# Performance work log

Measured on AMD Instinct MI355X. Metric: run time of the kernel, lower is better.

Reference implementation:

```python
import jax, jax.numpy as jnp
import numpy as np

# ---- st-moe constants (training-mode routing) ----
EPS = 1e-9
TOP_N = 2
CAP_FACTOR = 1.25      # capacity_factor_train
THRESHOLD = 0.2        # threshold_train (2nd expert)
BAL_COEF = 0.01
Z_COEF = 0.001
MIN_CAP = 4
LN_EPS = 1e-5

B, N, D, E = 4, 2048, 512, 8
H = int(D * 4 * 2 / 3)  # 1365, st-moe default Expert hidden


def _rms_norm(x, gamma):
    # F.normalize(x, dim=-1) * sqrt(d) * gamma
    nrm = jnp.maximum(jnp.linalg.norm(x, axis=-1, keepdims=True), 1e-12)
    return x / nrm * (x.shape[-1] ** 0.5) * gamma


def setup_inputs() -> dict:
    key = jax.random.key(0)
    ks = jax.random.split(key, 6)
    s = 0.02
    return {
        "x": jax.random.normal(ks[0], (B, N, D), jnp.float32),
        "gate_w": jax.random.normal(ks[1], (D, E), jnp.float32) * s,
        "prenorm_g": jnp.ones((D,), jnp.float32),
        "w1": jax.random.normal(ks[2], (E, D, 2 * H), jnp.float32) * s,
        "b1": jnp.zeros((E, 2 * H), jnp.float32),
        "mult_bias": jnp.ones((E, H), jnp.float32),
        "w2": jax.random.normal(ks[3], (E, H, D), jnp.float32) * s,
        "b2": jnp.zeros((E, D), jnp.float32),
        "ln_g": jnp.ones((D,), jnp.float32),
        "ln_b": jnp.zeros((D,), jnp.float32),
    }


def _stmoe_fnn(x, gate_w, prenorm_g, w1, b1, mult_bias, w2, b2, ln_g, ln_b):
    b, n, d = x.shape
    e = gate_w.shape[1]
    cap = max(MIN_CAP, min(n, int(n * CAP_FACTOR / e)))  # static python int

    # SparseMoEBlock: moe(RMSNorm(x)) + x
    xg = _rms_norm(x, prenorm_g)

    # ---- TopNGating ----
    gate_logits = jnp.einsum('bnd,de->bne', xg, gate_w)
    raw_gates = jax.nn.softmax(gate_logits, axis=-1)
    gates, idx = jax.lax.top_k(raw_gates, TOP_N)          # (b,n,k)
    gates = jnp.moveaxis(gates, -1, 0)                    # (k,b,n)
    idx = jnp.moveaxis(idx, -1, 0)                        # (k,b,n)
    one_hot = jax.nn.one_hot(idx, e, dtype=x.dtype)       # (k,b,n,e)

    denom = jnp.maximum(gates.sum(axis=0), EPS)
    gates = gates / denom                                 # normalized top-n scores

    # stochastic routing to non-first experts: prob = min(1, gate/threshold)
    thresh = jnp.array([EPS, THRESHOLD], x.dtype)[:, None, None]
    probs = jax.random.uniform(jax.random.key(42), gates.shape, x.dtype)
    should_route = probs < (gates / jnp.maximum(thresh, EPS))
    should_route = should_route.at[0].set(True)
    mask = one_hot * should_route[..., None].astype(x.dtype)  # (k,b,n,e)

    # exclusive cumsum over sequence -> position within each expert
    mask_cumsum = jnp.cumsum(mask, axis=-2) - mask

    positions, kept_masks = [], []
    prev_count = jnp.zeros((b, 1, e), x.dtype)
    for k in range(TOP_N):  # top_n=2, tiny static loop
        pos_in_expert = (mask_cumsum[k] + prev_count) * mask[k]      # (b,n,e)
        kept = mask[k] * (pos_in_expert < float(cap)).astype(x.dtype)
        prev_count = prev_count + kept.sum(axis=-2, keepdims=True)
        positions.append(pos_in_expert.sum(axis=-1))                 # (b,n)
        kept_masks.append(kept)
    mask = jnp.stack(kept_masks)       # (k,b,n,e) post-capacity
    positions = jnp.stack(positions)   # (k,b,n)

    mask_flat = mask.sum(axis=-1)      # (k,b,n)
    gates = gates * mask_flat

    # safe one-hot: out-of-range (overflow) positions map to all-zeros
    pos_one_hot = jax.nn.one_hot(positions.astype(jnp.int32), cap, dtype=x.dtype)  # (k,b,n,c)
    combine = jnp.einsum('kbn,kbne,kbnc->bnec', gates, one_hot, pos_one_hot)       # (b,n,e,c)

    # straight-through dispatch tensor
    dispatch = (combine > 0).astype(x.dtype) + combine - jax.lax.stop_gradient(combine)

    # ---- dispatch, expert GEGLU FFN, combine ----
    expert_in = jnp.einsum('bnd,bnec->becd', xg, dispatch)                 # (b,e,c,d)
    h = jnp.einsum('becd,edf->becf', expert_in, w1) + b1[None, :, None, :]
    u, g = jnp.split(h, 2, axis=-1)
    act = u * jax.nn.gelu(g, approximate=False) * mult_bias[None, :, None, :]
    expert_out = jnp.einsum('bech,ehd->becd', act, w2) + b2[None, :, None, :]
    moe_out = jnp.einsum('becd,bnec->bnd', expert_out, combine)

    # ---- aux losses (training mode) ----
    density_1 = mask[0].mean(axis=-2)          # (b,e), post-capacity mask (torch in-place view)
    density_proxy = raw_gates.mean(axis=-2)    # (b,e)
    balance_loss = (density_proxy * density_1).mean() * float(e ** 2)
    z = jax.nn.logsumexp(gate_logits, axis=-1)
    router_z_loss = jnp.mean(z * z)
    total_aux = BAL_COEF * balance_loss + Z_COEF * router_z_loss

    # residual, (dropout -> identity for determinism), LayerNorm
    y = moe_out + x
    mu = y.mean(axis=-1, keepdims=True)
    var = jnp.mean((y - mu) ** 2, axis=-1, keepdims=True)
    out = (y - mu) * jax.lax.rsqrt(var + LN_EPS) * ln_g + ln_b
    return out, total_aux


def reference(x, gate_w, prenorm_g, w1, b1, mult_bias, w2, b2, ln_g, ln_b):
    return _stmoe_fnn(x, gate_w, prenorm_g, w1, b1, mult_bias, w2, b2, ln_g, ln_b)
```

## Files before the change

kernel.cpp:

```cpp
#include <hip/hip_runtime.h>
#include <hip/hip_bf16.h>
#include <math.h>

#define BB 4
#define NN 2048
#define DD 512
#define EE 8
#define HH 1365
#define H2 2730
#define CAP 320
#define NT (BB*NN)
#define KP2 1408
#define NW1 2816
#define ME 1280
#define KS1 16
#define KS2 44

typedef __bf16 bf16_t;
typedef __bf16 bf16x4 __attribute__((ext_vector_type(4)));
typedef __bf16 bf16x8 __attribute__((ext_vector_type(8)));
typedef float f32x4 __attribute__((ext_vector_type(4)));

__device__ __forceinline__ float gelu_exact(float x){
    return 0.5f * x * (1.0f + erff(x * 0.70710678118654752f));
}
__device__ __forceinline__ void gl2lds16(const void* g, void* s){
    __builtin_amdgcn_global_load_lds((const __attribute__((address_space(1))) unsigned int*)g,
                                     (__attribute__((address_space(3))) unsigned int*)s,
                                     16, 0, 0);
}
__device__ __forceinline__ unsigned rotl32(unsigned x, int d){ return (x<<d)|(x>>(32-d)); }
__device__ __forceinline__ void tf_round(unsigned &x0, unsigned &x1, int r){
    x0 += x1; x1 = rotl32(x1, r); x1 ^= x0;
}
__device__ float threefry_u01_second(unsigned t){
    const unsigned ks0 = 0u, ks1 = 42u, ks2 = 0x1BD11BDAu ^ 42u;
    unsigned x0 = t, x1 = t + 8192u;
    x0 += ks0; x1 += ks1;
    tf_round(x0,x1,13); tf_round(x0,x1,15); tf_round(x0,x1,26); tf_round(x0,x1,6);
    x0 += ks1; x1 += ks2 + 1u;
    tf_round(x0,x1,17); tf_round(x0,x1,29); tf_round(x0,x1,16); tf_round(x0,x1,24);
    x0 += ks2; x1 += ks0 + 2u;
    tf_round(x0,x1,13); tf_round(x0,x1,15); tf_round(x0,x1,26); tf_round(x0,x1,6);
    x0 += ks0; x1 += ks1 + 3u;
    tf_round(x0,x1,17); tf_round(x0,x1,29); tf_round(x0,x1,16); tf_round(x0,x1,24);
    x0 += ks1; x1 += ks2 + 4u;
    tf_round(x0,x1,13); tf_round(x0,x1,15); tf_round(x0,x1,26); tf_round(x0,x1,6);
    x0 += ks2; x1 += ks0 + 5u;
    unsigned bits = (x1 >> 9) | 0x3f800000u;
    return __uint_as_float(bits) - 1.0f;
}

#define PREP_GATE  2048
#define PREP_W1    (PREP_GATE+1)
#define PREP_W2    (PREP_W1+11264)
__global__ void k_prep(const float* __restrict__ x, const float* __restrict__ png,
                       const float* __restrict__ gw,
                       const float* __restrict__ w1, const float* __restrict__ w2,
                       bf16_t* __restrict__ xgb, bf16_t* __restrict__ w1t, bf16_t* __restrict__ w2t,
                       int* __restrict__ tok_e0, int* __restrict__ tok_e1,
                       float* __restrict__ tok_g0, float* __restrict__ tok_g1,
                       int* __restrict__ tok_c0, int* __restrict__ tok_c1,
                       float* __restrict__ dpPart, float* __restrict__ z2Part,
                       unsigned* __restrict__ scanCnt){
    __shared__ float T[32][33];
    __shared__ float s_raw[4][EE];
    __shared__ float s_z2[4];
    int bid = blockIdx.x;
    if (bid < PREP_GATE){
        int wave = threadIdx.x >> 6;
        int lane = threadIdx.x & 63;
        int t = bid*4 + wave;
        const float* row = x + (size_t)t*DD;
        float xv[8]; float ss = 0.f;
        #pragma unroll
        for (int i=0;i<8;i++){ xv[i] = row[lane + i*64]; ss += xv[i]*xv[i]; }
        #pragma unroll
        for (int off=32; off; off>>=1) ss += __shfl_xor(ss, off);
        float scale = 22.62741699796952f / fmaxf(sqrtf(ss), 1e-12f);
        float acc[EE];
        #pragma unroll
        for (int e=0;e<EE;e++) acc[e]=0.f;
        #pragma unroll
        for (int i=0;i<8;i++){
            int k = lane + i*64;
            float v = xv[i] * scale * png[k];
            xgb[(size_t)t*DD + k] = (bf16_t)v;
            const float* w = gw + k*EE;
            #pragma unroll
            for (int e=0;e<EE;e++) acc[e] = fmaf(v, w[e], acc[e]);
        }
        #pragma unroll
        for (int off=32; off; off>>=1){
            #pragma unroll
            for (int e=0;e<EE;e++) acc[e] += __shfl_down(acc[e], off);
        }
        if (lane==0){
            float mx = acc[0];
            #pragma unroll
            for (int e=1;e<EE;e++) mx = fmaxf(mx, acc[e]);
            float p[EE]; float se=0.f;
            #pragma unroll
            for (int e=0;e<EE;e++){ p[e] = expf(acc[e]-mx); se += p[e]; }
            float inv = 1.f/se;
            #pragma unroll
            for (int e=0;e<EE;e++) p[e] *= inv;
            float z = mx + logf(se);
            int i0=0;
            #pragma unroll
            for (int e=1;e<EE;e++) if (p[e] > p[i0]) i0=e;
            int i1 = (i0==0)?1:0;
            #pragma unroll
            for (int e=0;e<EE;e++){ if (e==i0) continue; if (p[e] > p[i1]) i1=e; }
            float g0=p[i0], g1=p[i1];
            float denom = fmaxf(g0+g1, 1e-9f);
            g0/=denom; g1/=denom;
            float prob = threefry_u01_second((unsigned)t);
            bool route1 = prob < (g1 * 5.0f);
            tok_e0[t] = i0;
            tok_e1[t] = route1 ? i1 : -1;
            tok_g0[t] = g0;
            tok_g1[t] = g1;
            tok_c0[t] = -1;
            tok_c1[t] = -1;
            #pragma unroll
            for (int e=0;e<EE;e++) s_raw[wave][e] = p[e];
            s_z2[wave] = z*z;
        }
        __syncthreads();
        if (threadIdx.x < EE){
            float sum = s_raw[0][threadIdx.x]+s_raw[1][threadIdx.x]+s_raw[2][threadIdx.x]+s_raw[3][threadIdx.x];
            dpPart[threadIdx.x*(size_t)NN + bid] = sum;
        }
        if (threadIdx.x == EE) z2Part[bid] = s_z2[0]+s_z2[1]+s_z2[2]+s_z2[3];
    } else if (bid == PREP_GATE){
        xgb[(size_t)NT*DD + threadIdx.x]       = (bf16_t)0.f;
        xgb[(size_t)NT*DD + threadIdx.x + 256] = (bf16_t)0.f;
        if (threadIdx.x == 0) scanCnt[0] = 0u;
    } else if (bid < PREP_W2){
        int f = bid - PREP_W1;
        int n32 = f % 88;
        int ks  = (f / 88) % 16;
        int e   = f / 1408;
        int n0 = n32 * 32;
        int tx = threadIdx.x & 31;
        int tg = threadIdx.x >> 5;
        int n = n0 + tx;
        #pragma unroll
        for (int i=0;i<4;i++){
            int kk = tg + i*8;
            int k = ks*32 + kk;
            float v = 0.f;
            if (n < KP2){ if (n < HH) v = w1[((size_t)e*DD + k)*H2 + n]; }
            else { int h = n - KP2; if (h < HH) v = w1[((size_t)e*DD + k)*H2 + HH + h]; }
            T[kk][tx] = v;
        }
        __syncthreads();
        int rr = threadIdx.x >> 3, s = threadIdx.x & 7;
        bf16x4 o;
        #pragma unroll
        for (int j=0;j<4;j++) o[j] = (bf16_t)T[s*4+j][rr];
        size_t off = (((size_t)e*KS1 + ks)*NW1 + n0 + rr)*32 + s*4;
        *(bf16x4*)(w1t + off) = o;
    } else {
        int f = bid - PREP_W2;
        int d32 = f % 16;
        int ks  = (f / 16) % 44;
        int e   = f / 704;
        int n0 = d32 * 32;
        int tx = threadIdx.x & 31;
        int tg = threadIdx.x >> 5;
        #pragma unroll
        for (int i=0;i<4;i++){
            int kk = tg + i*8;
            int k = ks*32 + kk;
            float v = 0.f;
            if (k < HH) v = w2[((size_t)e*HH + k)*DD + n0 + tx];
            T[kk][tx] = v;
        }
        __syncthreads();
        int rr = threadIdx.x >> 3, s = threadIdx.x & 7;
        bf16x4 o;
        #pragma unroll
        for (int j=0;j<4;j++) o[j] = (bf16_t)T[s*4+j][rr];
        size_t off = (((size_t)e*KS2 + ks)*DD + n0 + rr)*32 + s*4;
        *(bf16x4*)(w2t + off) = o;
    }
}

__global__ void k_scan(const int* __restrict__ tok_e0, const int* __restrict__ tok_e1,
                       int* __restrict__ tok_c0, int* __restrict__ tok_c1,
                       int* __restrict__ slot_tok, int* __restrict__ kept0cnt,
                       const float* __restrict__ dpPart, const float* __restrict__ z2Part,
                       unsigned* __restrict__ scanCnt, float* __restrict__ out_aux){
    __shared__ int s[256];
    __shared__ float sdp[32][9];
    __shared__ float sz[256];
    __shared__ bool s_last;
    int be = blockIdx.x;
    int b = be >> 3, e = be & 7;
    int tid = threadIdx.x;
    int sbase = (e*BB + b)*CAP;
    for (int i=tid; i<CAP; i+=256) slot_tok[sbase + i] = -1;
    __syncthreads();
    int n0 = tid * 8;
    int base_t = b*NN;
    int m0=0, m1=0;
    for (int i=0;i<8;i++){
        int t = base_t + n0 + i;
        m0 += (tok_e0[t]==e);
        m1 += (tok_e1[t]==e);
    }
    s[tid] = m0 | (m1<<16);
    __syncthreads();
    for (int off=1; off<256; off<<=1){
        int v = 0;
        if (tid >= off) v = s[tid-off];
        __syncthreads();
        if (tid >= off) s[tid] += v;
        __syncthreads();
    }
    int incl = s[tid];
    int total = s[255];
    int p0 = (incl & 0xffff) - m0;
    int p1 = (incl >> 16) - m1;
    int t0 = total & 0xffff;
    int kept0 = min(t0, CAP);
    int c0 = p0, c1 = p1;
    for (int i=0;i<8;i++){
        int n = n0 + i;
        int t = base_t + n;
        if (tok_e0[t]==e){
            int pos = c0++;
            if (pos < CAP){ tok_c0[t] = pos; slot_tok[sbase + pos] = t; }
        }
        if (tok_e1[t]==e){
            int pos = kept0 + c1++;
            if (pos < CAP){ tok_c1[t] = pos; slot_tok[sbase + pos] = t; }
        }
    }
    if (tid==0) kept0cnt[be] = kept0;
    __threadfence();
    __syncthreads();
    if (tid==0){
        unsigned old = atomicAdd(scanCnt, 1u);
        s_last = (old == (unsigned)(BB*EE - 1));
    }
    __syncthreads();
    if (!s_last) return;
    __threadfence();
    float za = 0.f;
    for (int i=tid; i<NN; i+=256) za += z2Part[i];
    sz[tid] = za; __syncthreads();
    for (int off=128; off; off>>=1){ if (tid<off) sz[tid]+=sz[tid+off]; __syncthreads(); }
    int seg = tid >> 3, off8 = tid & 7;
    int bb2 = seg >> 3, ee2 = seg & 7;
    float a = 0.f;
    for (int j=off8; j<512; j+=8) a += dpPart[ee2*(size_t)NN + bb2*512 + j];
    sdp[seg][off8] = a;
    __syncthreads();
    if (tid == 0){
        float z2t = sz[0];
        float bal = 0.f;
        for (int sgi=0; sgi<32; sgi++){
            float d = 0.f;
            #pragma unroll
            for (int k=0;k<8;k++) d += sdp[sgi][k];
            float d1 = (float)kept0cnt[sgi] / (float)NN;
            bal += (d / (float)NN) * d1;
        }
        bal = bal / 32.f * 64.f;
        out_aux[0] = 0.01f * bal + 0.001f * (z2t / (float)NT);
    }
}

__global__ __launch_bounds__(512,2) void k_ffn1_mfma(
    const bf16_t* __restrict__ xgb, const bf16_t* __restrict__ w1t,
    const float* __restrict__ b1, const float* __restrict__ mbias,
    const int* __restrict__ slot_tok, bf16_t* __restrict__ actb)
{
    int bid = blockIdx.x;
    int e = bid & 7;
    int r = bid >> 3;
    int mblk = r % 5, hb = r / 5;
    int lane = threadIdx.x & 63, wave = threadIdx.x >> 6;
    int quad = lane >> 4, col = lane & 15;
    int wm = wave & 3, wn = wave >> 2;

    __shared__ __align__(16) bf16_t sA[16*512];
    __shared__ __align__(16) bf16_t sBu[8*512];
    __shared__ __align__(16) bf16_t sBg[8*512];

    const bf16_t* gsrc[4];
    bf16_t* sdst[4];
    int gstep[4];
    const size_t w1t_e = (size_t)e*KS1*NW1*32;
    #pragma unroll
    for (int i=0;i<4;i++){
        int id = wave + 8*i;
        if (id < 16){
            int m = mblk*256 + id*16 + col;
            int slot = slot_tok[e*ME + m];
            int row = (slot >= 0) ? slot : NT;
            gsrc[i] = xgb + (size_t)row*DD + quad*8;
            sdst[i] = sA + id*512;
            gstep[i] = 32;
        } else if (id < 24){
            int n = hb*128 + (id-16)*16 + col;
            gsrc[i] = w1t + w1t_e + (size_t)n*32 + quad*8;
            sdst[i] = sBu + (id-16)*512;
            gstep[i] = NW1*32;
        } else {
            int n = KP2 + hb*128 + (id-24)*16 + col;
            gsrc[i] = w1t + w1t_e + (size_t)n*32 + quad*8;
            sdst[i] = sBg + (id-24)*512;
            gstep[i] = NW1*32;
        }
    }

    f32x4 accU[4][4], accG[4][4];
    #pragma unroll
    for (int mi=0;mi<4;mi++)
        #pragma unroll
        for (int ni=0;ni<4;ni++){
            accU[mi][ni] = (f32x4){0.f,0.f,0.f,0.f};
            accG[mi][ni] = (f32x4){0.f,0.f,0.f,0.f};
        }

    for (int ks=0; ks<KS1; ks++){
        #pragma unroll
        for (int i=0;i<4;i++){ gl2lds16(gsrc[i], sdst[i]); gsrc[i] += gstep[i]; }
        __syncthreads();
        bf16x8 a[4], bu[4], bg[4];
        #pragma unroll
        for (int mi=0;mi<4;mi++) a[mi] = *(const bf16x8*)(sA + (wm*4+mi)*512 + lane*8);
        #pragma unroll
        for (int ni=0;ni<4;ni++){
            bu[ni] = *(const bf16x8*)(sBu + (wn*4+ni)*512 + lane*8);
            bg[ni] = *(const bf16x8*)(sBg + (wn*4+ni)*512 + lane*8);
        }
        #pragma unroll
        for (int mi=0;mi<4;mi++)
            #pragma unroll
            for (int ni=0;ni<4;ni++){
                accU[mi][ni] = __builtin_amdgcn_mfma_f32_16x16x32_bf16(a[mi], bu[ni], accU[mi][ni], 0,0,0);
                accG[mi][ni] = __builtin_amdgcn_mfma_f32_16x16x32_bf16(a[mi], bg[ni], accG[mi][ni], 0,0,0);
            }
        __syncthreads();
    }

    const size_t actb_e = (size_t)e*KS2*ME*32;
    #pragma unroll
    for (int ni=0; ni<4; ni++){
        int h = hb*128 + wn*64 + ni*16 + col;
        bool valid = (h < HH);
        float bu_ = valid ? b1[e*H2 + h] : 0.f;
        float bg_ = valid ? b1[e*H2 + HH + h] : 0.f;
        float mb_ = valid ? mbias[e*HH + h] : 0.f;
        int ks2 = h >> 5, kl = h & 31;
        #pragma unroll
        for (int mi=0; mi<4; mi++){
            int m = mblk*256 + wm*64 + mi*16 + quad*4;
            bf16_t* base = actb + actb_e + ((size_t)ks2*ME + m)*32 + kl;
            #pragma unroll
            for (int rr=0; rr<4; rr++){
                float v = 0.f;
                if (valid){
                    float u = accU[mi][ni][rr] + bu_;
                    float g = accG[mi][ni][rr] + bg_;
                    v = u * gelu_exact(g) * mb_;
                }
                base[rr*32] = (bf16_t)v;
            }
        }
    }
}

__global__ __launch_bounds__(256,4) void k_ffn2_mfma(
    const bf16_t* __restrict__ actb, const bf16_t* __restrict__ w2t,
    bf16_t* __restrict__ eoA, bf16_t* __restrict__ eoB)
{
    int bid = blockIdx.x;
    int e = bid & 7;
    int r = bid >> 3;
    int mblk = r % 10;
    int q = r / 10;
    int db = q & 3, kh = q >> 2;
    int lane = threadIdx.x & 63, wave = threadIdx.x >> 6;
    int quad = lane >> 4, col = lane & 15;
    int wx = wave & 1, wy = wave >> 1;

    __shared__ __align__(16) bf16_t sA[8*512];
    __shared__ __align__(16) bf16_t sB[8*512];

    const bf16_t* gsrc[4];
    bf16_t* sdst[4];
    int gstep[4];
    const size_t actb_e = (size_t)e*KS2*ME*32 + (size_t)(kh*22)*ME*32;
    const size_t w2t_e  = (size_t)e*KS2*DD*32 + (size_t)(kh*22)*DD*32;
    #pragma unroll
    for (int i=0;i<4;i++){
        int id = wave + 4*i;
        if (id < 8){
            int m = mblk*128 + id*16 + col;
            gsrc[i] = actb + actb_e + (size_t)m*32 + quad*8;
            sdst[i] = sA + id*512;
            gstep[i] = ME*32;
        } else {
            int d = db*128 + (id-8)*16 + col;
            gsrc[i] = w2t + w2t_e + (size_t)d*32 + quad*8;
            sdst[i] = sB + (id-8)*512;
            gstep[i] = DD*32;
        }
    }

    f32x4 acc[4][4];
    #pragma unroll
    for (int mi=0;mi<4;mi++)
        #pragma unroll
        for (int ni=0;ni<4;ni++) acc[mi][ni] = (f32x4){0.f,0.f,0.f,0.f};

    for (int ks=0; ks<22; ks++){
        #pragma unroll
        for (int i=0;i<4;i++){ gl2lds16(gsrc[i], sdst[i]); gsrc[i] += gstep[i]; }
        __syncthreads();
        bf16x8 a[4], bv[4];
        #pragma unroll
        for (int mi=0;mi<4;mi++) a[mi] = *(const bf16x8*)(sA + (wx*4+mi)*512 + lane*8);
        #pragma unroll
        for (int ni=0;ni<4;ni++) bv[ni] = *(const bf16x8*)(sB + (wy*4+ni)*512 + lane*8);
        #pragma unroll
        for (int mi=0;mi<4;mi++)
            #pragma unroll
            for (int ni=0;ni<4;ni++)
                acc[mi][ni] = __builtin_amdgcn_mfma_f32_16x16x32_bf16(a[mi], bv[ni], acc[mi][ni], 0,0,0);
        __syncthreads();
    }

    bf16_t* eop = kh ? eoB : eoA;
    #pragma unroll
    for (int ni=0; ni<4; ni++){
        int d = db*128 + wy*64 + ni*16 + col;
        #pragma unroll
        for (int mi=0; mi<4; mi++){
            int m = mblk*128 + wx*64 + mi*16 + quad*4;
            #pragma unroll
            for (int rr=0; rr<4; rr++)
                eop[((size_t)e*ME + m + rr)*DD + d] = (bf16_t)acc[mi][ni][rr];
        }
    }
}

__global__ void k_combine(const float* __restrict__ x,
        const bf16_t* __restrict__ eoA, const bf16_t* __restrict__ eoB,
        const int* __restrict__ tok_e0, const int* __restrict__ tok_e1,
        const int* __restrict__ tok_c0, const int* __restrict__ tok_c1,
        const float* __restrict__ tok_g0, const float* __restrict__ tok_g1,
        const float* __restrict__ b2,
        const float* __restrict__ ln_g, const float* __restrict__ ln_b,
        float* __restrict__ out){
    int t = blockIdx.x;
    int b = t / NN;
    int tid = threadIdx.x;
    int i4 = tid*4;
    int e0 = tok_e0[t], c0 = tok_c0[t];
    int e1 = tok_e1[t], c1 = tok_c1[t];
    float g0 = tok_g0[t], g1 = tok_g1[t];
    float4 xv = *(const float4*)(x + (size_t)t*DD + i4);
    float v[4] = {xv.x, xv.y, xv.z, xv.w};
    if (c0 >= 0){
        size_t idx = ((size_t)(e0*ME + b*CAP + c0))*DD + i4;
        bf16x4 pa = *(const bf16x4*)(eoA + idx);
        bf16x4 pb = *(const bf16x4*)(eoB + idx);
        float4 bb = *(const float4*)(b2 + e0*DD + i4);
        v[0] += g0 * ((float)pa[0] + (float)pb[0] + bb.x);
        v[1] += g0 * ((float)pa[1] + (float)pb[1] + bb.y);
        v[2] += g0 * ((float)pa[2] + (float)pb[2] + bb.z);
        v[3] += g0 * ((float)pa[3] + (float)pb[3] + bb.w);
    }
    if (e1 >= 0 && c1 >= 0){
        size_t idx = ((size_t)(e1*ME + b*CAP + c1))*DD + i4;
        bf16x4 pa = *(const bf16x4*)(eoA + idx);
        bf16x4 pb = *(const bf16x4*)(eoB + idx);
        float4 bb = *(const float4*)(b2 + e1*DD + i4);
        v[0] += g1 * ((float)pa[0] + (float)pb[0] + bb.x);
        v[1] += g1 * ((float)pa[1] + (float)pb[1] + bb.y);
        v[2] += g1 * ((float)pa[2] + (float)pb[2] + bb.z);
        v[3] += g1 * ((float)pa[3] + (float)pb[3] + bb.w);
    }
    float s = v[0]+v[1]+v[2]+v[3];
    float s2 = v[0]*v[0]+v[1]*v[1]+v[2]*v[2]+v[3]*v[3];
    __shared__ float rs[2], rs2[2];
    #pragma unroll
    for (int off=32; off; off>>=1){ s += __shfl_down(s,off); s2 += __shfl_down(s2,off); }
    if ((tid&63)==0){ rs[tid>>6]=s; rs2[tid>>6]=s2; }
    __syncthreads();
    float mu  = (rs[0]+rs[1]) * (1.0f/512.0f);
    float var = (rs2[0]+rs2[1]) * (1.0f/512.0f) - mu*mu;
    float inv = rsqrtf(var + 1e-5f);
    float4 gv = *(const float4*)(ln_g + i4);
    float4 bv = *(const float4*)(ln_b + i4);
    float4 o;
    o.x = (v[0]-mu)*inv*gv.x + bv.x;
    o.y = (v[1]-mu)*inv*gv.y + bv.y;
    o.z = (v[2]-mu)*inv*gv.z + bv.z;
    o.w = (v[3]-mu)*inv*gv.w + bv.w;
    *(float4*)(out + (size_t)t*DD + i4) = o;
}

extern "C" void kernel_launch(void* const* d_in, const int* in_sizes, int n_in,
                              void* d_out, int out_size, void* d_ws, size_t ws_size,
                              hipStream_t stream) {
    const float* x         = (const float*)d_in[0];
    const float* gate_w    = (const float*)d_in[1];
    const float* prenorm_g = (const float*)d_in[2];
    const float* w1        = (const float*)d_in[3];
    const float* b1        = (const float*)d_in[4];
    const float* mult_bias = (const float*)d_in[5];
    const float* w2        = (const float*)d_in[6];
    const float* b2        = (const float*)d_in[7];
    const float* ln_g      = (const float*)d_in[8];
    const float* ln_b      = (const float*)d_in[9];
    float* out = (float*)d_out;

    char* p = (char*)d_ws;
    bf16_t* xgb = (bf16_t*)p; p += (size_t)(NT+1)*DD*2;
    bf16_t* w1t = (bf16_t*)p; p += (size_t)EE*KS1*NW1*32*2;
    bf16_t* w2t = (bf16_t*)p; p += (size_t)EE*KS2*DD*32*2;
    bf16_t* actb = (bf16_t*)p; p += (size_t)EE*KS2*ME*32*2;
    bf16_t* eoA = (bf16_t*)p; p += (size_t)EE*ME*DD*2;
    bf16_t* eoB = (bf16_t*)p; p += (size_t)EE*ME*DD*2;
    int* slot_tok = (int*)p; p += EE*BB*CAP*4;
    int* tok_e0 = (int*)p; p += NT*4;
    int* tok_e1 = (int*)p; p += NT*4;
    int* tok_c0 = (int*)p; p += NT*4;
    int* tok_c1 = (int*)p; p += NT*4;
    float* tok_g0 = (float*)p; p += NT*4;
    float* tok_g1 = (float*)p; p += NT*4;
    float* dpPart = (float*)p; p += EE*NN*4;
    float* z2Part = (float*)p; p += NN*4;
    int* kept0 = (int*)p; p += BB*EE*4;
    unsigned* scanCnt = (unsigned*)p; p += 4;

    k_prep<<<PREP_W2 + 5632, 256, 0, stream>>>(x, prenorm_g, gate_w, w1, w2,
                                               xgb, w1t, w2t,
                                               tok_e0, tok_e1, tok_g0, tok_g1,
                                               tok_c0, tok_c1, dpPart, z2Part, scanCnt);
    k_scan<<<BB*EE, 256, 0, stream>>>(tok_e0, tok_e1, tok_c0, tok_c1, slot_tok, kept0,
                                      dpPart, z2Part, scanCnt, out + (size_t)NT*DD);
    k_ffn1_mfma<<<EE*5*11, 512, 0, stream>>>(xgb, w1t, b1, mult_bias, slot_tok, actb);
    k_ffn2_mfma<<<EE*10*4*2, 256, 0, stream>>>(actb, w2t, eoA, eoB);
    k_combine<<<NT, 128, 0, stream>>>(x, eoA, eoB, tok_e0, tok_e1, tok_c0, tok_c1,
                                      tok_g0, tok_g1, b2, ln_g, ln_b, out);
}
```

Measured before the change: 269.1 us.

## Move w2 transpose into FFN1 launch and shrink FFN1 tiles to 128x128

```diff
diff --git a/kernel.cpp b/kernel.cpp
--- a/kernel.cpp
+++ b/kernel.cpp
@@ -53,11 +53,11 @@
 
 #define PREP_GATE  2048
 #define PREP_W1    (PREP_GATE+1)
-#define PREP_W2    (PREP_W1+11264)
+#define PREP_END   (PREP_W1+11264)
 __global__ void k_prep(const float* __restrict__ x, const float* __restrict__ png,
                        const float* __restrict__ gw,
-                       const float* __restrict__ w1, const float* __restrict__ w2,
-                       bf16_t* __restrict__ xgb, bf16_t* __restrict__ w1t, bf16_t* __restrict__ w2t,
+                       const float* __restrict__ w1,
+                       bf16_t* __restrict__ xgb, bf16_t* __restrict__ w1t,
                        int* __restrict__ tok_e0, int* __restrict__ tok_e1,
                        float* __restrict__ tok_g0, float* __restrict__ tok_g1,
                        int* __restrict__ tok_c0, int* __restrict__ tok_c1,
@@ -137,7 +137,7 @@
         xgb[(size_t)NT*DD + threadIdx.x]       = (bf16_t)0.f;
         xgb[(size_t)NT*DD + threadIdx.x + 256] = (bf16_t)0.f;
         if (threadIdx.x == 0) scanCnt[0] = 0u;
-    } else if (bid < PREP_W2){
+    } else {
         int f = bid - PREP_W1;
         int n32 = f % 88;
         int ks  = (f / 88) % 16;
@@ -162,29 +162,6 @@
         for (int j=0;j<4;j++) o[j] = (bf16_t)T[s*4+j][rr];
         size_t off = (((size_t)e*KS1 + ks)*NW1 + n0 + rr)*32 + s*4;
         *(bf16x4*)(w1t + off) = o;
-    } else {
-        int f = bid - PREP_W2;
-        int d32 = f % 16;
-        int ks  = (f / 16) % 44;
-        int e   = f / 704;
-        int n0 = d32 * 32;
-        int tx = threadIdx.x & 31;
-        int tg = threadIdx.x >> 5;
-        #pragma unroll
-        for (int i=0;i<4;i++){
-            int kk = tg + i*8;
-            int k = ks*32 + kk;
-            float v = 0.f;
-            if (k < HH) v = w2[((size_t)e*HH + k)*DD + n0 + tx];
-            T[kk][tx] = v;
-        }
-        __syncthreads();
-        int rr = threadIdx.x >> 3, s = threadIdx.x & 7;
-        bf16x4 o;
-        #pragma unroll
-        for (int j=0;j<4;j++) o[j] = (bf16_t)T[s*4+j][rr];
-        size_t off = (((size_t)e*KS2 + ks)*DD + n0 + rr)*32 + s*4;
-        *(bf16x4*)(w2t + off) = o;
     }
 }
 
@@ -274,46 +251,73 @@
     }
 }
 
-__global__ __launch_bounds__(512,2) void k_ffn1_mfma(
+__global__ __launch_bounds__(256,2) void k_ffn1_mfma(
     const bf16_t* __restrict__ xgb, const bf16_t* __restrict__ w1t,
     const float* __restrict__ b1, const float* __restrict__ mbias,
-    const int* __restrict__ slot_tok, bf16_t* __restrict__ actb)
+    const int* __restrict__ slot_tok, bf16_t* __restrict__ actb,
+    const float* __restrict__ w2, bf16_t* __restrict__ w2t)
 {
+    __shared__ __align__(16) bf16_t sA[8*512];
+    __shared__ __align__(16) bf16_t sB[16*512];
     int bid = blockIdx.x;
+
+    if (bid >= 880){
+        float (*T)[33] = (float(*)[33])sA;
+        int f = bid - 880;
+        int d32 = f & 15;
+        int ks  = (f >> 4) % 44;
+        int e   = f / 704;
+        int n0 = d32 * 32;
+        int tx = threadIdx.x & 31;
+        int tg = threadIdx.x >> 5;
+        #pragma unroll
+        for (int i=0;i<4;i++){
+            int kk = tg + i*8;
+            int k = ks*32 + kk;
+            float v = 0.f;
+            if (k < HH) v = w2[((size_t)e*HH + k)*DD + n0 + tx];
+            T[kk][tx] = v;
+        }
+        __syncthreads();
+        int rr = threadIdx.x >> 3, s = threadIdx.x & 7;
+        bf16x4 o;
+        #pragma unroll
+        for (int j=0;j<4;j++) o[j] = (bf16_t)T[s*4+j][rr];
+        size_t off = (((size_t)e*KS2 + ks)*DD + n0 + rr)*32 + s*4;
+        *(bf16x4*)(w2t + off) = o;
+        return;
+    }
+
     int e = bid & 7;
     int r = bid >> 3;
-    int mblk = r % 5, hb = r / 5;
+    int mblk = r % 10, hb = r / 10;
     int lane = threadIdx.x & 63, wave = threadIdx.x >> 6;
     int quad = lane >> 4, col = lane & 15;
-    int wm = wave & 3, wn = wave >> 2;
-
-    __shared__ __align__(16) bf16_t sA[16*512];
-    __shared__ __align__(16) bf16_t sBu[8*512];
-    __shared__ __align__(16) bf16_t sBg[8*512];
-
-    const bf16_t* gsrc[4];
-    bf16_t* sdst[4];
-    int gstep[4];
+    int wx = wave & 1, wy = wave >> 1;
+
+    const bf16_t* gsrc[6];
+    bf16_t* sdst[6];
+    int gstep[6];
     const size_t w1t_e = (size_t)e*KS1*NW1*32;
     #pragma unroll
-    for (int i=0;i<4;i++){
-        int id = wave + 8*i;
-        if (id < 16){
-            int m = mblk*256 + id*16 + col;
+    for (int i=0;i<6;i++){
+        int id = wave + 4*i;
+        if (id < 8){
+            int m = mblk*128 + id*16 + col;
             int slot = slot_tok[e*ME + m];
             int row = (slot >= 0) ? slot : NT;
             gsrc[i] = xgb + (size_t)row*DD + quad*8;
             sdst[i] = sA + id*512;
             gstep[i] = 32;
-        } else if (id < 24){
-            int n = hb*128 + (id-16)*16 + col;
+        } else if (id < 16){
+            int n = hb*128 + (id-8)*16 + col;
             gsrc[i] = w1t + w1t_e + (size_t)n*32 + quad*8;
-            sdst[i] = sBu + (id-16)*512;
+            sdst[i] = sB + (id-8)*512;
             gstep[i] = NW1*32;
         } else {
-            int n = KP2 + hb*128 + (id-24)*16 + col;
+            int n = KP2 + hb*128 + (id-16)*16 + col;
             gsrc[i] = w1t + w1t_e + (size_t)n*32 + quad*8;
-            sdst[i] = sBg + (id-24)*512;
+            sdst[i] = sB + (id-8)*512;
             gstep[i] = NW1*32;
         }
     }
@@ -329,15 +333,15 @@
 
     for (int ks=0; ks<KS1; ks++){
         #pragma unroll
-        for (int i=0;i<4;i++){ gl2lds16(gsrc[i], sdst[i]); gsrc[i] += gstep[i]; }
+        for (int i=0;i<6;i++){ gl2lds16(gsrc[i], sdst[i]); gsrc[i] += gstep[i]; }
         __syncthreads();
         bf16x8 a[4], bu[4], bg[4];
         #pragma unroll
-        for (int mi=0;mi<4;mi++) a[mi] = *(const bf16x8*)(sA + (wm*4+mi)*512 + lane*8);
+        for (int mi=0;mi<4;mi++) a[mi] = *(const bf16x8*)(sA + (wx*4+mi)*512 + lane*8);
         #pragma unroll
         for (int ni=0;ni<4;ni++){
-            bu[ni] = *(const bf16x8*)(sBu + (wn*4+ni)*512 + lane*8);
-            bg[ni] = *(const bf16x8*)(sBg + (wn*4+ni)*512 + lane*8);
+            bu[ni] = *(const bf16x8*)(sB + (wy*4+ni)*512 + lane*8);
+            bg[ni] = *(const bf16x8*)(sB + (8+wy*4+ni)*512 + lane*8);
         }
         #pragma unroll
         for (int mi=0;mi<4;mi++)
@@ -352,7 +356,7 @@
     const size_t actb_e = (size_t)e*KS2*ME*32;
     #pragma unroll
     for (int ni=0; ni<4; ni++){
-        int h = hb*128 + wn*64 + ni*16 + col;
+        int h = hb*128 + wy*64 + ni*16 + col;
         bool valid = (h < HH);
         float bu_ = valid ? b1[e*H2 + h] : 0.f;
         float bg_ = valid ? b1[e*H2 + HH + h] : 0.f;
@@ -360,7 +364,7 @@
         int ks2 = h >> 5, kl = h & 31;
         #pragma unroll
         for (int mi=0; mi<4; mi++){
-            int m = mblk*256 + wm*64 + mi*16 + quad*4;
+            int m = mblk*128 + wx*64 + mi*16 + quad*4;
             bf16_t* base = actb + actb_e + ((size_t)ks2*ME + m)*32 + kl;
             #pragma unroll
             for (int rr=0; rr<4; rr++){
@@ -376,7 +380,7 @@
     }
 }
 
-__global__ __launch_bounds__(256,4) void k_ffn2_mfma(
+__global__ __launch_bounds__(256,3) void k_ffn2_mfma(
     const bf16_t* __restrict__ actb, const bf16_t* __restrict__ w2t,
     bf16_t* __restrict__ eoA, bf16_t* __restrict__ eoB)
 {
@@ -542,13 +546,14 @@
     int* kept0 = (int*)p; p += BB*EE*4;
     unsigned* scanCnt = (unsigned*)p; p += 4;
 
-    k_prep<<<PREP_W2 + 5632, 256, 0, stream>>>(x, prenorm_g, gate_w, w1, w2,
-                                               xgb, w1t, w2t,
-                                               tok_e0, tok_e1, tok_g0, tok_g1,
-                                               tok_c0, tok_c1, dpPart, z2Part, scanCnt);
+    k_prep<<<PREP_END, 256, 0, stream>>>(x, prenorm_g, gate_w, w1,
+                                         xgb, w1t,
+                                         tok_e0, tok_e1, tok_g0, tok_g1,
+                                         tok_c0, tok_c1, dpPart, z2Part, scanCnt);
     k_scan<<<BB*EE, 256, 0, stream>>>(tok_e0, tok_e1, tok_c0, tok_c1, slot_tok, kept0,
                                       dpPart, z2Part, scanCnt, out + (size_t)NT*DD);
-    k_ffn1_mfma<<<EE*5*11, 512, 0, stream>>>(xgb, w1t, b1, mult_bias, slot_tok, actb);
+    k_ffn1_mfma<<<880 + 5632, 256, 0, stream>>>(xgb, w1t, b1, mult_bias, slot_tok, actb,
+                                                w2, w2t);
     k_ffn2_mfma<<<EE*10*4*2, 256, 0, stream>>>(actb, w2t, eoA, eoB);
     k_combine<<<NT, 128, 0, stream>>>(x, eoA, eoB, tok_e0, tok_e1, tok_c0, tok_c1,
                                       tok_g0, tok_g1, b2, ln_g, ln_b, out);
```

After: 271.3 us. No clear change (+0.8%).
